# Performance work log

Measured on AMD Instinct MI355X. Metric: run time of the kernel, lower is better.

Reference implementation:

```python
import jax, jax.numpy as jnp
import numpy as np

N_NODES = 50000
N_EDGES = 1600000
IN_CH = 129   # encoding_dim + node_dim
OUT_CH = 64
PERIODS = 25
N_TRAIN = 25000


def setup_inputs() -> dict:
    key = jax.random.key(0)
    ks = jax.random.split(key, 24)
    inp = {
        'x': jax.random.normal(ks[0], (N_NODES, IN_CH, PERIODS), dtype=jnp.float32),
        'edge_index': jax.random.randint(ks[1], (2, N_EDGES), 0, N_NODES, dtype=jnp.int64),
        'y': jax.random.uniform(ks[2], (N_NODES,), dtype=jnp.float32),
        'train_idx': jax.random.randint(ks[3], (N_TRAIN,), 0, N_NODES, dtype=jnp.int64),
    }
    s_in = 1.0 / np.sqrt(IN_CH)
    s_2o = 1.0 / np.sqrt(2 * OUT_CH)
    s_o = 1.0 / np.sqrt(OUT_CH)
    # TGCN gate params: GCNConv weight/bias (IN_CH->OUT_CH), Linear(2*OUT_CH->OUT_CH)
    names = ['z', 'r', 'h']
    for i, g in enumerate(names):
        inp[f'W_{g}'] = jax.random.uniform(ks[4 + 4 * i], (IN_CH, OUT_CH), minval=-s_in, maxval=s_in)
        inp[f'b_{g}'] = jax.random.uniform(ks[5 + 4 * i], (OUT_CH,), minval=-s_in, maxval=s_in)
        inp[f'Wl_{g}'] = jax.random.uniform(ks[6 + 4 * i], (2 * OUT_CH, OUT_CH), minval=-s_2o, maxval=s_2o)
        inp[f'bl_{g}'] = jax.random.uniform(ks[7 + 4 * i], (OUT_CH,), minval=-s_2o, maxval=s_2o)
    inp['attention'] = jax.random.uniform(ks[16], (PERIODS,), dtype=jnp.float32)
    inp['W_o'] = jax.random.uniform(ks[17], (OUT_CH, 1), minval=-s_o, maxval=s_o)
    inp['b_o'] = jax.random.uniform(ks[18], (1,), minval=-s_o, maxval=s_o)
    return inp


def _forward(x, edge_index, y, train_idx, attention,
             W_z, b_z, Wl_z, bl_z, W_r, b_r, Wl_r, bl_r,
             W_h, b_h, Wl_h, bl_h, W_o, b_o):
    N = x.shape[0]
    src, dst = edge_index[0], edge_index[1]
    # GCN symmetric norm with self-loops (edge_weight = 1)
    deg = 1.0 + jax.ops.segment_sum(jnp.ones_like(src, dtype=x.dtype), dst, num_segments=N)
    dinv = jax.lax.rsqrt(deg)
    edge_norm = (dinv[src] * dinv[dst])[:, None]   # (E,1)
    self_norm = (dinv * dinv)[:, None]              # (N,1)

    def gcn(xt, W, b):
        h = xt @ W                                   # (N, OUT_CH)
        agg = jax.ops.segment_sum(edge_norm * h[src], dst, num_segments=N)
        return agg + self_norm * h + b

    probs = jax.nn.softmax(attention)               # (PERIODS,)
    x_seq = jnp.transpose(x, (2, 0, 1))             # (T, N, IN_CH)

    def step(carry, xp):
        H, acc = carry
        xt, p = xp
        Z = jax.nn.sigmoid(jnp.concatenate([gcn(xt, W_z, b_z), H], axis=1) @ Wl_z + bl_z)
        R = jax.nn.sigmoid(jnp.concatenate([gcn(xt, W_r, b_r), H], axis=1) @ Wl_r + bl_r)
        H_tilde = jnp.tanh(jnp.concatenate([gcn(xt, W_h, b_h), H * R], axis=1) @ Wl_h + bl_h)
        H = Z * H + (1.0 - Z) * H_tilde
        return (H, acc + p * H), None

    H0 = jnp.zeros((N, OUT_CH), dtype=x.dtype)
    (H, H_accum), _ = jax.lax.scan(step, (H0, H0), (x_seq, probs))

    out = jax.nn.sigmoid(H_accum @ W_o + b_o)       # (N, 1)
    y_pred = out[:, 0][train_idx]
    return y_pred, y[train_idx]


def reference(x, edge_index, y, train_idx, attention,
              W_z, b_z, Wl_z, bl_z, W_r, b_r, Wl_r, bl_r,
              W_h, b_h, Wl_h, bl_h, W_o, b_o):
    return _forward(x, edge_index, y, train_idx, attention,
                    W_z, b_z, Wl_z, bl_z, W_r, b_r, Wl_r, bl_r,
                    W_h, b_h, Wl_h, bl_h, W_o, b_o)
```

## Files before the change

kernel.cpp:

```cpp
#include <hip/hip_runtime.h>
#include <stdint.h>

#define NND 50000
#define NNDP 50016
#define NE  1600000
#define INC 129
#define TP  25
#define NTR 25000
#define MPAD 50048
#define NC 192
#define NB_SCAN 196
#define CSR_MAX (NE + 8*NND + 128)

typedef short bf16x8 __attribute__((ext_vector_type(8)));
typedef float f32x4 __attribute__((ext_vector_type(4)));
typedef float f32x2 __attribute__((ext_vector_type(2)));

__device__ __forceinline__ uint32_t f2bf(float f){
  union{float ff; uint32_t u;} v; v.ff=f;
  return (v.u + 0x7FFFu + ((v.u>>16)&1u))>>16;
}
__device__ __forceinline__ uint32_t pack2(float a, float b){
  return f2bf(a) | (f2bf(b)<<16);
}
__device__ __forceinline__ float sigm(float v){ return 1.f/(1.f+__expf(-v)); }

__global__ void k_prep(const float* Wz, const float* bz, const float* Wlz, const float* blz,
                       const float* Wr, const float* br, const float* Wlr, const float* blr,
                       const float* Wh, const float* bh, const float* Wlh, const float* blh,
                       uint16_t* BT, float* ceff, uint16_t* WlhT)
{
  int idx = blockIdx.x*256 + threadIdx.x;
  if (idx < NC*224) {
    int j = idx / 224, k = idx - j*224;
    int g = j >> 6, jj = j & 63;
    const float* W  = g==0?Wz :(g==1?Wr :Wh);
    const float* Wl = g==0?Wlz:(g==1?Wlr:Wlh);
    float v = 0.f;
    if (k < INC) {
      for (int m=0;m<64;m++) v += W[k*64+m]*Wl[m*64+jj];
    } else if (k >= 160) {
      int kk = k-160;
      v = (g<2) ? Wl[(64+kk)*64 + jj] : 0.f;
    }
    BT[idx] = (uint16_t)f2bf(v);
  } else if (idx < NC*224 + 64*64) {
    int t = idx - NC*224; int j = t>>6, k = t&63;
    WlhT[t] = (uint16_t)f2bf(Wlh[(64+k)*64 + j]);
  } else if (idx < NC*224 + 64*64 + NC) {
    int j = idx - NC*224 - 64*64;
    int g = j>>6, jj = j&63;
    const float* b  = g==0?bz :(g==1?br :bh);
    const float* Wl = g==0?Wlz:(g==1?Wlr:Wlh);
    const float* bl = g==0?blz:(g==1?blr:blh);
    float v = bl[jj];
    for (int m=0;m<64;m++) v += b[m]*Wl[m*64+jj];
    ceff[j] = v;
  }
}

__global__ void k_probs(const float* att, float* probs){
  if (threadIdx.x==0 && blockIdx.x==0){
    float m=-1e30f;
    for (int i=0;i<TP;i++) m = fmaxf(m, att[i]);
    float e[TP]; float s=0.f;
    for (int i=0;i<TP;i++){ e[i]=__expf(att[i]-m); s+=e[i]; }
    for (int i=0;i<TP;i++) probs[i]=e[i]/s;
  }
}

__global__ void k_hist(const int* eidx, int* deg){
  int e = blockIdx.x*256 + threadIdx.x;
  if (e < NE) atomicAdd(&deg[eidx[NE + e]], 1);
}

__global__ void k_dinv(const int* deg, float* dinv){
  int n = blockIdx.x*256 + threadIdx.x;
  if (n < NND) dinv[n] = rsqrtf(1.0f + (float)deg[n]);
}

__global__ void k_scan1(const int* deg, int* row_ptr, int* bsum){
  __shared__ int s[256];
  int tid = threadIdx.x;
  int i = blockIdx.x*256 + tid;
  int v = (i < NND) ? ((deg[i]+8)&~7) : 0;
  s[tid] = v; __syncthreads();
  for (int d=1; d<256; d<<=1){
    int t = (tid>=d) ? s[tid-d] : 0;
    __syncthreads();
    s[tid] += t; __syncthreads();
  }
  if (i < NND) row_ptr[i] = s[tid] - v;
  if (tid == 255) bsum[blockIdx.x] = s[255];
}
__global__ void k_scan2(int* bsum, int* boff, int* row_ptr){
  __shared__ int s[256];
  int tid = threadIdx.x;
  int v = (tid < NB_SCAN) ? bsum[tid] : 0;
  s[tid] = v; __syncthreads();
  for (int d=1; d<256; d<<=1){
    int t = (tid>=d) ? s[tid-d] : 0;
    __syncthreads();
    s[tid] += t; __syncthreads();
  }
  if (tid < NB_SCAN) boff[tid] = s[tid] - v;
  if (tid == NB_SCAN-1) row_ptr[NND] = s[tid];
}
__global__ void k_scan3(int* row_ptr, const int* boff){
  int i = blockIdx.x*256 + threadIdx.x;
  if (i < NND) row_ptr[i] += boff[blockIdx.x];
}

__global__ void k_fill(const int* eidx, const int* rp, int* cnt, uint16_t* csr){
  int e = blockIdx.x*256 + threadIdx.x;
  if (e < NE){
    int s = eidx[e], d = eidx[NE+e];
    int pos = rp[d] + atomicAdd(&cnt[d],1);
    csr[pos] = (uint16_t)s;
  }
}
__global__ void k_self(const int* rp, const int* deg, uint16_t* csr){
  int n = blockIdx.x*256 + threadIdx.x;
  if (n < NND){
    int base = rp[n] + deg[n];
    int endp = rp[n+1];
    csr[base] = (uint16_t)n;
    for (int j=base+1; j<endp; j++) csr[j] = (uint16_t)NND;
  }
}

__global__ __launch_bounds__(256) void k_transpose3(const float* __restrict__ x,
                                                    const float* __restrict__ dinv,
                                                    uint32_t* __restrict__ xT8,
                                                    float* __restrict__ xsl){
  __shared__ float lx[3232];
  int n = blockIdx.x;
  const float* xr = x + (size_t)n*(INC*TP);
  for (int e=threadIdx.x; e<INC*TP; e+=256) lx[e] = xr[e];
  __syncthreads();
  float dv = dinv[n];
  for (int idx=threadIdx.x; idx<TP*32; idx+=256){
    int t = idx>>5, u = idx&31;
    int c0 = u*4;
    float v0 = lx[(c0+0)*TP+t]*dv, v1 = lx[(c0+1)*TP+t]*dv;
    float v2 = lx[(c0+2)*TP+t]*dv, v3 = lx[(c0+3)*TP+t]*dv;
    int wlo = __builtin_amdgcn_cvt_pk_fp8_f32(v0, v1, 0, false);
    int w   = __builtin_amdgcn_cvt_pk_fp8_f32(v2, v3, wlo, true);
    xT8[((size_t)t*NNDP + n)*32 + u] = (uint32_t)w;
  }
  for (int t=threadIdx.x; t<TP; t+=256)
    xsl[(size_t)t*NNDP + n] = dv*lx[128*TP + t];
  if (blockIdx.x == 0){
    for (int idx=threadIdx.x; idx<TP*32; idx+=256){
      int t = idx>>5, u = idx&31;
      xT8[((size_t)t*NNDP + NND)*32 + u] = 0u;
    }
    for (int t=threadIdx.x; t<TP; t+=256) xsl[(size_t)t*NNDP + NND] = 0.f;
  }
}

__global__ __launch_bounds__(256) void k_agg(const uint16_t* __restrict__ xT8,
    const int* __restrict__ rp, const uint16_t* __restrict__ csr,
    const float* __restrict__ dinv, uint32_t* __restrict__ AX)
{
  int t = blockIdx.y;
  int wave = threadIdx.x>>6, lane = threadIdx.x&63;
  int d = blockIdx.x*4 + wave;
  int beg = __builtin_amdgcn_readfirstlane(rp[d]);
  int end = __builtin_amdgcn_readfirstlane(rp[d+1]);
  const uint16_t* tbl = xT8 + (size_t)t*((size_t)NNDP*64);
  float a0=0.f, a1=0.f;
  for (int i0=beg; i0<end; i0+=8){
    ulonglong2 c = *(const ulonglong2*)(csr + i0);
    #pragma unroll
    for (int k=0;k<4;k++){
      int s0 = (int)((c.x >> (k*16)) & 0xFFFFu);
      int s1 = (int)((c.y >> (k*16)) & 0xFFFFu);
      uint32_t u0 = tbl[(size_t)s0*64 + lane];
      uint32_t u1 = tbl[(size_t)s1*64 + lane];
      f32x2 v0 = __builtin_amdgcn_cvt_pk_f32_fp8((int)u0, false);
      f32x2 v1 = __builtin_amdgcn_cvt_pk_f32_fp8((int)u1, false);
      a0 += v0.x; a1 += v0.y;
      a0 += v1.x; a1 += v1.y;
    }
  }
  float dv = dinv[d];
  AX[(size_t)t*((size_t)MPAD*80) + (size_t)d*80 + lane] = pack2(dv*a0, dv*a1);
}

__global__ void k_aggL(const float* __restrict__ xsl,
    const int* __restrict__ rp, const uint16_t* __restrict__ csr,
    const float* __restrict__ dinv, uint32_t* __restrict__ AX)
{
  int t = blockIdx.y;
  int d = blockIdx.x*256 + threadIdx.x;
  if (d >= NND) return;
  const float* pl = xsl + (size_t)t*NNDP;
  float a = 0.f;
  int beg=rp[d], end=rp[d+1];
  #pragma unroll 4
  for (int i=beg;i<end;i++) a += pl[(int)csr[i]];
  AX[(size_t)t*((size_t)MPAD*80) + (size_t)d*80 + 64] = pack2(dinv[d]*a, 0.f);
}

__global__ __launch_bounds__(256) void k_gru(const uint32_t* __restrict__ AX,
    const uint32_t* __restrict__ BT, const float* __restrict__ ceff,
    const uint32_t* __restrict__ WlhTu, float* __restrict__ accum,
    const float* __restrict__ probs)
{
  __shared__ __align__(16) uint32_t lA[64*116];
  __shared__ __align__(16) uint32_t lB[64*116];
  uint32_t* lW = lA;
  uint16_t* lHR = (uint16_t*)lB;
  uint16_t* lAh = (uint16_t*)lA;
  int tid = threadIdx.x;
  int n0 = blockIdx.x*64;
  int wave=tid>>6, lane=tid&63;
  int col16 = lane&15, kgrp = lane>>4;
  int arow = wave*16 + col16;
  int rbase = wave*16 + kgrp*4;

  for (int idx=tid; idx<64*32; idx+=256){
    int r=idx>>5, cu=idx&31;
    lA[r*116 + 80 + cu] = 0u;
  }

  f32x4 h[4] = {{0,0,0,0},{0,0,0,0},{0,0,0,0},{0,0,0,0}};
  f32x4 acr[4] = {{0,0,0,0},{0,0,0,0},{0,0,0,0},{0,0,0,0}};

  for (int t=0; t<TP; t++){
    const uint32_t* AXt = AX + (size_t)t*((size_t)MPAD*80);
    __syncthreads();
    for (int idx=tid; idx<64*80; idx+=256){
      int r = idx/80, cu = idx - r*80;
      lA[r*116+cu] = AXt[(size_t)(n0+r)*80 + cu];
    }
    for (int idx=tid; idx<64*112; idx+=256){
      int r = idx/112, cu = idx - r*112;
      lB[r*116+cu] = BT[(size_t)r*112 + cu];
    }
    __syncthreads();

    f32x4 accg[3][4] = {};
    #pragma unroll
    for (int g=0; g<3; g++){
      #pragma unroll
      for (int kk=0; kk<7; kk++){
        bf16x8 a = *(const bf16x8*)&lA[arow*116 + kk*16 + kgrp*4];
        #pragma unroll
        for (int cc=0; cc<4; cc++){
          bf16x8 b = *(const bf16x8*)&lB[(cc*16 + col16)*116 + kk*16 + kgrp*4];
          accg[g][cc] = __builtin_amdgcn_mfma_f32_16x16x32_bf16(a,b,accg[g][cc],0,0,0);
        }
      }
      if (g<2){
        __syncthreads();
        for (int idx=tid; idx<64*112; idx+=256){
          int r = idx/112, cu = idx - r*112;
          lB[r*116+cu] = BT[(size_t)(g+1)*64*112 + (size_t)r*112 + cu];
        }
        __syncthreads();
      }
    }
    __syncthreads();

    #pragma unroll
    for (int cc=0;cc<4;cc++){
      #pragma unroll
      for (int j=0;j<4;j++){
        int rl = rbase + j;
        int jl = cc*16 + col16;
        float z  = sigm(accg[0][cc][j] + ceff[jl]);
        float r  = sigm(accg[1][cc][j] + ceff[64+jl]);
        float ph = accg[2][cc][j] + ceff[128+jl];
        accg[0][cc][j] = z;
        accg[2][cc][j] = ph;
        lHR[rl*88 + jl] = (uint16_t)f2bf(h[cc][j]*r);
      }
    }
    for (int idx=tid; idx<64*32; idx+=256){
      int r=idx>>5, cu=idx&31;
      lW[r*36+cu] = WlhTu[r*32+cu];
    }
    __syncthreads();

    f32x4 acc2[4] = {};
    #pragma unroll
    for (int kk=0;kk<2;kk++){
      bf16x8 a = *(const bf16x8*)&lHR[arow*88 + kk*32 + kgrp*8];
      #pragma unroll
      for (int cc=0;cc<4;cc++){
        bf16x8 b = *(const bf16x8*)&lW[(cc*16+col16)*36 + kk*16 + kgrp*4];
        acc2[cc]=__builtin_amdgcn_mfma_f32_16x16x32_bf16(a,b,acc2[cc],0,0,0);
      }
    }

    float pt = probs[t];
    #pragma unroll
    for (int cc=0;cc<4;cc++){
      #pragma unroll
      for (int j=0;j<4;j++){
        int rl = rbase + j;
        int jl = cc*16+col16;
        float ht = tanhf(acc2[cc][j] + accg[2][cc][j]);
        float z = accg[0][cc][j];
        float hn = z*h[cc][j] + (1.f-z)*ht;
        h[cc][j] = hn;
        acr[cc][j] += pt*hn;
        lAh[rl*232 + 160 + jl] = (uint16_t)f2bf(hn);
      }
    }
  }

  #pragma unroll
  for (int cc=0;cc<4;cc++){
    #pragma unroll
    for (int j=0;j<4;j++){
      int n = n0 + rbase + j;
      if (n < NND)
        accum[(size_t)n*64 + cc*16 + col16] = acr[cc][j];
    }
  }
}

__global__ void k_out(const int* train_idx, const float* accum, const float* Wo,
                      const float* bo, const float* y, float* out){
  int i = blockIdx.x*256 + threadIdx.x;
  if (i < NTR){
    int n = train_idx[i];
    float s = bo[0];
    const float* ar = accum + (size_t)n*64;
    #pragma unroll
    for (int j=0;j<64;j++) s += ar[j]*Wo[j];
    out[i] = sigm(s);
    out[NTR+i] = y[n];
  }
}

extern "C" void kernel_launch(void* const* d_in, const int* in_sizes, int n_in,
                              void* d_out, int out_size, void* d_ws, size_t ws_size,
                              hipStream_t stream)
{
  const float* x   = (const float*)d_in[0];
  const int*   eix = (const int*)d_in[1];
  const float* y   = (const float*)d_in[2];
  const int*   tri = (const int*)d_in[3];
  const float* Wz  = (const float*)d_in[4];
  const float* bz  = (const float*)d_in[5];
  const float* Wlz = (const float*)d_in[6];
  const float* blz = (const float*)d_in[7];
  const float* Wr  = (const float*)d_in[8];
  const float* br  = (const float*)d_in[9];
  const float* Wlr = (const float*)d_in[10];
  const float* blr = (const float*)d_in[11];
  const float* Wh  = (const float*)d_in[12];
  const float* bh  = (const float*)d_in[13];
  const float* Wlh = (const float*)d_in[14];
  const float* blh = (const float*)d_in[15];
  const float* att = (const float*)d_in[16];
  const float* Wo  = (const float*)d_in[17];
  const float* bo  = (const float*)d_in[18];
  float* out = (float*)d_out;

  char* w = (char*)d_ws;
  size_t off = 0;
  auto alloc = [&](size_t sz)->size_t{ size_t o=off; off=(off+sz+255)&~(size_t)255; return o; };

  size_t zo = off;
  size_t o_deg   = alloc((size_t)NND*4);
  size_t o_cnt   = alloc((size_t)NND*4);
  size_t zlen = off - zo;
  size_t o_dinv  = alloc((size_t)NND*4);
  size_t o_rp    = alloc((size_t)(NND+1)*4);
  size_t o_bsum  = alloc((size_t)NB_SCAN*4);
  size_t o_boff  = alloc((size_t)NB_SCAN*4);
  size_t o_csr   = alloc((size_t)CSR_MAX*2);
  size_t o_BT    = alloc((size_t)NC*224*2);
  size_t o_ceff  = alloc((size_t)NC*4);
  size_t o_WlhT  = alloc((size_t)64*64*2);
  size_t o_probs = alloc((size_t)TP*4);
  size_t o_accum = alloc((size_t)MPAD*64*4);
  size_t o_AX    = alloc((size_t)TP*MPAD*80*4);
  size_t o_xT8   = alloc((size_t)TP*NNDP*128);
  size_t o_xl    = alloc((size_t)TP*NNDP*4);
  (void)ws_size; (void)in_sizes; (void)n_in; (void)out_size;

  int*      deg   = (int*)(w+o_deg);
  int*      cnt   = (int*)(w+o_cnt);
  float*    dinv  = (float*)(w+o_dinv);
  int*      rp    = (int*)(w+o_rp);
  int*      bsum  = (int*)(w+o_bsum);
  int*      boff  = (int*)(w+o_boff);
  uint16_t* csr   = (uint16_t*)(w+o_csr);
  uint16_t* BT    = (uint16_t*)(w+o_BT);
  float*    ceff  = (float*)(w+o_ceff);
  uint16_t* WlhT  = (uint16_t*)(w+o_WlhT);
  float*    probs = (float*)(w+o_probs);
  float*    accum = (float*)(w+o_accum);
  uint32_t* AX    = (uint32_t*)(w+o_AX);
  uint32_t* xT8   = (uint32_t*)(w+o_xT8);
  float*    xsl   = (float*)(w+o_xl);

  hipMemsetAsync(w+zo, 0, zlen, stream);

  k_prep<<<(NC*224 + 64*64 + NC + 255)/256, 256, 0, stream>>>(
      Wz,bz,Wlz,blz, Wr,br,Wlr,blr, Wh,bh,Wlh,blh, BT, ceff, WlhT);
  k_probs<<<1, 64, 0, stream>>>(att, probs);
  k_hist<<<(NE+255)/256, 256, 0, stream>>>(eix, deg);
  k_dinv<<<(NND+255)/256, 256, 0, stream>>>(deg, dinv);
  k_scan1<<<NB_SCAN, 256, 0, stream>>>(deg, rp, bsum);
  k_scan2<<<1, 256, 0, stream>>>(bsum, boff, rp);
  k_scan3<<<NB_SCAN, 256, 0, stream>>>(rp, boff);
  k_fill<<<(NE+255)/256, 256, 0, stream>>>(eix, rp, cnt, csr);
  k_self<<<NB_SCAN, 256, 0, stream>>>(rp, deg, csr);
  k_transpose3<<<NND, 256, 0, stream>>>(x, dinv, xT8, xsl);

  k_agg <<<dim3(12500, TP), 256, 0, stream>>>((const uint16_t*)xT8, rp, csr, dinv, AX);
  k_aggL<<<dim3(NB_SCAN, TP), 256, 0, stream>>>(xsl, rp, csr, dinv, AX);

  k_gru<<<MPAD/64, 256, 0, stream>>>(AX, (const uint32_t*)BT, ceff,
                                     (const uint32_t*)WlhT, accum, probs);
  k_out<<<(NTR+255)/256, 256, 0, stream>>>(tri, accum, Wo, bo, y, out);
}
```

Baseline: 1.928 ms.

## Pre-swizzle GRU weights into MFMA fragment order and drop block-wide LDS staging

The gate weight matrices are now written by the prep kernel directly in the per-lane MFMA B-fragment order, so k_gru reads them straight from global/L2 with one vector load per fragment. This replaces the repeated LDS staging of weights and the many __syncthreads per timestep. AX rows are likewise loaded straight into registers. Hidden state and H*R are kept in small per-wave LDS regions in fragment order, built with lane shuffles and packed bf16 stores. Block-wide barriers go away, at the cost of more global weight traffic per wave, which relies on cache hits.

```diff
diff --git a/kernel.cpp b/kernel.cpp
--- a/kernel.cpp
+++ b/kernel.cpp
@@ -28,7 +28,7 @@
 __global__ void k_prep(const float* Wz, const float* bz, const float* Wlz, const float* blz,
                        const float* Wr, const float* br, const float* Wlr, const float* blr,
                        const float* Wh, const float* bh, const float* Wlh, const float* blh,
-                       uint16_t* BT, float* ceff, uint16_t* WlhT)
+                       uint16_t* BTf, float* ceff, uint16_t* Wlf)
 {
   int idx = blockIdx.x*256 + threadIdx.x;
   if (idx < NC*224) {
@@ -43,10 +43,16 @@
       int kk = k-160;
       v = (g<2) ? Wl[(64+kk)*64 + jj] : 0.f;
     }
-    BT[idx] = (uint16_t)f2bf(v);
+    int cc = (j>>4)&3, c16 = j&15;
+    int kd = k>>1, kk = kd>>4, kgrp = (kd>>2)&3, dw = kd&3, half = k&1;
+    int lane = kgrp*16 + c16;
+    BTf[(((g*7+kk)*4+cc)*256 + lane*4 + dw)*2 + half] = (uint16_t)f2bf(v);
   } else if (idx < NC*224 + 64*64) {
-    int t = idx - NC*224; int j = t>>6, k = t&63;
-    WlhT[t] = (uint16_t)f2bf(Wlh[(64+k)*64 + j]);
+    int t = idx - NC*224; int j2 = t>>6, k2 = t&63;
+    int cc = j2>>4, c16 = j2&15;
+    int kd = k2>>1, kk2 = kd>>4, kgrp = (kd>>2)&3, dw = kd&3, half = k2&1;
+    int lane = kgrp*16 + c16;
+    Wlf[((kk2*4+cc)*256 + lane*4 + dw)*2 + half] = (uint16_t)f2bf(Wlh[(64+k2)*64 + j2]);
   } else if (idx < NC*224 + 64*64 + NC) {
     int j = idx - NC*224 - 64*64;
     int g = j>>6, jj = j&63;
@@ -204,94 +210,80 @@
 }
 
 __global__ __launch_bounds__(256) void k_gru(const uint32_t* __restrict__ AX,
-    const uint32_t* __restrict__ BT, const float* __restrict__ ceff,
-    const uint32_t* __restrict__ WlhTu, float* __restrict__ accum,
+    const uint32_t* __restrict__ BTf, const float* __restrict__ ceff,
+    const uint32_t* __restrict__ Wlf, float* __restrict__ accum,
     const float* __restrict__ probs)
 {
-  __shared__ __align__(16) uint32_t lA[64*116];
-  __shared__ __align__(16) uint32_t lB[64*116];
-  uint32_t* lW = lA;
-  uint16_t* lHR = (uint16_t*)lB;
-  uint16_t* lAh = (uint16_t*)lA;
+  __shared__ __align__(16) uint32_t lds4[4*1024];
   int tid = threadIdx.x;
+  int wave = tid>>6, lane = tid&63;
+  int col16 = lane&15, kgrp = lane>>4;
+  uint32_t* myH  = &lds4[wave*1024];
+  uint32_t* myHR = &lds4[wave*1024 + 512];
   int n0 = blockIdx.x*64;
-  int wave=tid>>6, lane=tid&63;
-  int col16 = lane&15, kgrp = lane>>4;
-  int arow = wave*16 + col16;
-  int rbase = wave*16 + kgrp*4;
-
-  for (int idx=tid; idx<64*32; idx+=256){
-    int r=idx>>5, cu=idx&31;
-    lA[r*116 + 80 + cu] = 0u;
+
+  for (int p=lane; p<512; p+=64) myH[p] = 0u;
+
+  float cz[4], cr[4], ch[4];
+  #pragma unroll
+  for (int cc=0;cc<4;cc++){
+    cz[cc] = ceff[cc*16+col16];
+    cr[cc] = ceff[64+cc*16+col16];
+    ch[cc] = ceff[128+cc*16+col16];
   }
 
   f32x4 h[4] = {{0,0,0,0},{0,0,0,0},{0,0,0,0},{0,0,0,0}};
   f32x4 acr[4] = {{0,0,0,0},{0,0,0,0},{0,0,0,0},{0,0,0,0}};
 
   for (int t=0; t<TP; t++){
-    const uint32_t* AXt = AX + (size_t)t*((size_t)MPAD*80);
-    __syncthreads();
-    for (int idx=tid; idx<64*80; idx+=256){
-      int r = idx/80, cu = idx - r*80;
-      lA[r*116+cu] = AXt[(size_t)(n0+r)*80 + cu];
-    }
-    for (int idx=tid; idx<64*112; idx+=256){
-      int r = idx/112, cu = idx - r*112;
-      lB[r*116+cu] = BT[(size_t)r*112 + cu];
-    }
-    __syncthreads();
+    const uint32_t* AXrow = AX + (size_t)t*((size_t)MPAD*80)
+                               + (size_t)(n0 + wave*16 + col16)*80 + kgrp*4;
+    bf16x8 ax[5];
+    #pragma unroll
+    for (int kk=0; kk<5; kk++) ax[kk] = *(const bf16x8*)(AXrow + kk*16);
+    bf16x8 hf0 = *(const bf16x8*)&myH[lane*4];
+    bf16x8 hf1 = *(const bf16x8*)&myH[256 + lane*4];
 
     f32x4 accg[3][4] = {};
     #pragma unroll
     for (int g=0; g<3; g++){
       #pragma unroll
       for (int kk=0; kk<7; kk++){
-        bf16x8 a = *(const bf16x8*)&lA[arow*116 + kk*16 + kgrp*4];
+        bf16x8 a = (kk<5) ? ax[kk] : ((kk==5) ? hf0 : hf1);
         #pragma unroll
         for (int cc=0; cc<4; cc++){
-          bf16x8 b = *(const bf16x8*)&lB[(cc*16 + col16)*116 + kk*16 + kgrp*4];
+          bf16x8 b = *(const bf16x8*)(BTf + (((g*7+kk)*4+cc)<<8) + lane*4);
           accg[g][cc] = __builtin_amdgcn_mfma_f32_16x16x32_bf16(a,b,accg[g][cc],0,0,0);
         }
       }
-      if (g<2){
-        __syncthreads();
-        for (int idx=tid; idx<64*112; idx+=256){
-          int r = idx/112, cu = idx - r*112;
-          lB[r*116+cu] = BT[(size_t)(g+1)*64*112 + (size_t)r*112 + cu];
-        }
-        __syncthreads();
-      }
-    }
-    __syncthreads();
+    }
 
     #pragma unroll
     for (int cc=0;cc<4;cc++){
       #pragma unroll
       for (int j=0;j<4;j++){
-        int rl = rbase + j;
-        int jl = cc*16 + col16;
-        float z  = sigm(accg[0][cc][j] + ceff[jl]);
-        float r  = sigm(accg[1][cc][j] + ceff[64+jl]);
-        float ph = accg[2][cc][j] + ceff[128+jl];
+        float z  = sigm(accg[0][cc][j] + cz[cc]);
+        float r  = sigm(accg[1][cc][j] + cr[cc]);
+        float ph = accg[2][cc][j] + ch[cc];
         accg[0][cc][j] = z;
         accg[2][cc][j] = ph;
-        lHR[rl*88 + jl] = (uint16_t)f2bf(h[cc][j]*r);
+        float hr = h[cc][j]*r;
+        float prt = __shfl_xor(hr, 1);
+        if (!(col16 & 1)){
+          int q = cc*8 + (col16>>1);
+          myHR[((q>>4)<<8) + ((((q>>2)&3)*16 + kgrp*4 + j)<<2) + (q&3)] = pack2(hr, prt);
+        }
       }
     }
-    for (int idx=tid; idx<64*32; idx+=256){
-      int r=idx>>5, cu=idx&31;
-      lW[r*36+cu] = WlhTu[r*32+cu];
-    }
-    __syncthreads();
 
     f32x4 acc2[4] = {};
     #pragma unroll
-    for (int kk=0;kk<2;kk++){
-      bf16x8 a = *(const bf16x8*)&lHR[arow*88 + kk*32 + kgrp*8];
+    for (int kk2=0; kk2<2; kk2++){
+      bf16x8 a2 = *(const bf16x8*)&myHR[(kk2<<8) + lane*4];
       #pragma unroll
-      for (int cc=0;cc<4;cc++){
-        bf16x8 b = *(const bf16x8*)&lW[(cc*16+col16)*36 + kk*16 + kgrp*4];
-        acc2[cc]=__builtin_amdgcn_mfma_f32_16x16x32_bf16(a,b,acc2[cc],0,0,0);
+      for (int cc=0; cc<4; cc++){
+        bf16x8 b2 = *(const bf16x8*)(Wlf + (((kk2*4+cc))<<8) + lane*4);
+        acc2[cc] = __builtin_amdgcn_mfma_f32_16x16x32_bf16(a2,b2,acc2[cc],0,0,0);
       }
     }
 
@@ -300,14 +292,16 @@
     for (int cc=0;cc<4;cc++){
       #pragma unroll
       for (int j=0;j<4;j++){
-        int rl = rbase + j;
-        int jl = cc*16+col16;
         float ht = tanhf(acc2[cc][j] + accg[2][cc][j]);
         float z = accg[0][cc][j];
         float hn = z*h[cc][j] + (1.f-z)*ht;
         h[cc][j] = hn;
         acr[cc][j] += pt*hn;
-        lAh[rl*232 + 160 + jl] = (uint16_t)f2bf(hn);
+        float prt = __shfl_xor(hn, 1);
+        if (!(col16 & 1)){
+          int q = cc*8 + (col16>>1);
+          myH[((q>>4)<<8) + ((((q>>2)&3)*16 + kgrp*4 + j)<<2) + (q&3)] = pack2(hn, prt);
+        }
       }
     }
   }
@@ -316,7 +310,7 @@
   for (int cc=0;cc<4;cc++){
     #pragma unroll
     for (int j=0;j<4;j++){
-      int n = n0 + rbase + j;
+      int n = n0 + wave*16 + kgrp*4 + j;
       if (n < NND)
         accum[(size_t)n*64 + cc*16 + col16] = acr[cc][j];
     }
@@ -377,7 +371,7 @@
   size_t o_csr   = alloc((size_t)CSR_MAX*2);
   size_t o_BT    = alloc((size_t)NC*224*2);
   size_t o_ceff  = alloc((size_t)NC*4);
-  size_t o_WlhT  = alloc((size_t)64*64*2);
+  size_t o_Wlf   = alloc((size_t)64*64*2);
   size_t o_probs = alloc((size_t)TP*4);
   size_t o_accum = alloc((size_t)MPAD*64*4);
   size_t o_AX    = alloc((size_t)TP*MPAD*80*4);
@@ -392,9 +386,9 @@
   int*      bsum  = (int*)(w+o_bsum);
   int*      boff  = (int*)(w+o_boff);
   uint16_t* csr   = (uint16_t*)(w+o_csr);
-  uint16_t* BT    = (uint16_t*)(w+o_BT);
+  uint16_t* BTf   = (uint16_t*)(w+o_BT);
   float*    ceff  = (float*)(w+o_ceff);
-  uint16_t* WlhT  = (uint16_t*)(w+o_WlhT);
+  uint16_t* Wlf   = (uint16_t*)(w+o_Wlf);
   float*    probs = (float*)(w+o_probs);
   float*    accum = (float*)(w+o_accum);
   uint32_t* AX    = (uint32_t*)(w+o_AX);
@@ -404,7 +398,7 @@
   hipMemsetAsync(w+zo, 0, zlen, stream);
 
   k_prep<<<(NC*224 + 64*64 + NC + 255)/256, 256, 0, stream>>>(
-      Wz,bz,Wlz,blz, Wr,br,Wlr,blr, Wh,bh,Wlh,blh, BT, ceff, WlhT);
+      Wz,bz,Wlz,blz, Wr,br,Wlr,blr, Wh,bh,Wlh,blh, BTf, ceff, Wlf);
   k_probs<<<1, 64, 0, stream>>>(att, probs);
   k_hist<<<(NE+255)/256, 256, 0, stream>>>(eix, deg);
   k_dinv<<<(NND+255)/256, 256, 0, stream>>>(deg, dinv);
@@ -418,7 +412,7 @@
   k_agg <<<dim3(12500, TP), 256, 0, stream>>>((const uint16_t*)xT8, rp, csr, dinv, AX);
   k_aggL<<<dim3(NB_SCAN, TP), 256, 0, stream>>>(xsl, rp, csr, dinv, AX);
 
-  k_gru<<<MPAD/64, 256, 0, stream>>>(AX, (const uint32_t*)BT, ceff,
-                                     (const uint32_t*)WlhT, accum, probs);
+  k_gru<<<MPAD/64, 256, 0, stream>>>(AX, (const uint32_t*)BTf, ceff,
+                                     (const uint32_t*)Wlf, accum, probs);
   k_out<<<(NTR+255)/256, 256, 0, stream>>>(tri, accum, Wo, bo, y, out);
 }
```

After: 1.932 ms. No clear change (+0.2%).
